# Optimization experiments

Measured on AMD Instinct MI355X. Metric: run time of the kernel, lower is better.

Reference implementation:

```python
import jax, jax.numpy as jnp
import numpy as np
import math

B, S, H, D = 4, 2048, 16, 64
HID = H * D  # 1024


def setup_inputs() -> dict:
    key = jax.random.key(0)
    ks = jax.random.split(key, 9)
    s_in = 1.0 / math.sqrt(D)
    s_hid = 1.0 / math.sqrt(HID)
    return {
        "x": jax.random.normal(ks[0], (B, S, D), dtype=jnp.float32),
        "Wq": jax.random.uniform(ks[1], (D, HID), jnp.float32, -s_in, s_in),
        "bq": jax.random.uniform(ks[2], (HID,), jnp.float32, -s_in, s_in),
        "Wk": jax.random.uniform(ks[3], (D, HID), jnp.float32, -s_in, s_in),
        "bk": jax.random.uniform(ks[4], (HID,), jnp.float32, -s_in, s_in),
        "Wv": jax.random.uniform(ks[5], (D, HID), jnp.float32, -s_in, s_in),
        "bv": jax.random.uniform(ks[6], (HID,), jnp.float32, -s_in, s_in),
        "Wo": jax.random.uniform(ks[7], (HID, D), jnp.float32, -s_hid, s_hid),
        "bo": jax.random.uniform(ks[8], (D,), jnp.float32, -s_hid, s_hid),
    }


def reference(x, Wq, bq, Wk, bk, Wv, bv, Wo, bo):
    b, s, _ = x.shape
    # projections: [B,S,D] -> [B,S,HID] -> [B,H,S,D]
    q = (x @ Wq + bq).reshape(b, s, H, D).transpose(0, 2, 1, 3)
    k = (x @ Wk + bk).reshape(b, s, H, D).transpose(0, 2, 1, 3)
    v = (x @ Wv + bv).reshape(b, s, H, D).transpose(0, 2, 1, 3)
    scores = jnp.einsum("bhqd,bhkd->bhqk", q, k) / math.sqrt(D)
    # causal mask: -inf strictly above the diagonal
    causal = jnp.tril(jnp.ones((s, s), dtype=bool))
    scores = jnp.where(causal, scores, -jnp.inf)
    attn = jax.nn.softmax(scores, axis=-1)  # dropout is identity at eval
    out = jnp.einsum("bhqk,bhkd->bhqd", attn, v)
    out = out.transpose(0, 2, 1, 3).reshape(b, s, HID)
    return out @ Wo + bo  # [B,S,D]
```

## Files before the change

kernel.cpp:

```cpp
#include <hip/hip_runtime.h>
#include <hip/hip_bf16.h>

#define B 4
#define S 2048
#define H 16
#define D 64
#define HID 1024

typedef __hip_bfloat16 bf16;
typedef __attribute__((ext_vector_type(8))) short bf16x8;
typedef __attribute__((ext_vector_type(4))) short bf16x4;
typedef __attribute__((ext_vector_type(4))) float f32x4;

static __device__ __forceinline__ float b2f(bf16 v) { return __bfloat162float(v); }

static __device__ __forceinline__ unsigned pkbf(float a, float b) {
    union { bf16 h; unsigned short u; } ua, ub;
    ua.h = __float2bfloat16(a);
    ub.h = __float2bfloat16(b);
    return (unsigned)ua.u | ((unsigned)ub.u << 16);
}

#define SCL 0.18033688011112042f

#define QSTR 72
#define VTS  132

__global__ __launch_bounds__(256) void qkv_mfma_kernel(
    const float* __restrict__ x,
    const float* __restrict__ Wq, const float* __restrict__ bq,
    const float* __restrict__ Wk, const float* __restrict__ bk,
    const float* __restrict__ Wv, const float* __restrict__ bv,
    bf16* __restrict__ q, bf16* __restrict__ k, bf16* __restrict__ v)
{
    __shared__ __align__(16) char smem[36864];
    __shared__ float bs[128];
    bf16* Xs = (bf16*)smem;
    bf16* Wt = (bf16*)(smem + 128 * QSTR * 2);

    const int tid = threadIdx.x;
    const int mat = blockIdx.y >> 3;
    const int N0  = (blockIdx.y & 7) * 128;
    const int m0  = blockIdx.x * 128;

    const float* W    = (mat == 0) ? Wq : (mat == 1) ? Wk : Wv;
    const float* bias = (mat == 0) ? bq : (mat == 1) ? bk : bv;
    bf16*        dst  = (mat == 0) ? q  : (mat == 1) ? k  : v;
    const float  oscale = (mat == 0) ? SCL : 1.0f;

    #pragma unroll
    for (int i = 0; i < 8; ++i) {
        int item = i * 256 + tid;
        int row = item >> 4, f4 = item & 15;
        float4 xv = *(const float4*)&x[(size_t)(m0 + row) * D + f4 * 4];
        union { bf16 h[4]; bf16x4 v4; } u;
        u.h[0] = __float2bfloat16(xv.x); u.h[1] = __float2bfloat16(xv.y);
        u.h[2] = __float2bfloat16(xv.z); u.h[3] = __float2bfloat16(xv.w);
        *(bf16x4*)&Xs[row * QSTR + f4 * 4] = u.v4;
    }
    #pragma unroll
    for (int i = 0; i < 2; ++i) {
        int unit = i * 256 + tid;
        int n0 = (unit & 31) * 4, k0 = (unit >> 5) * 4;
        float wv[4][4];
        #pragma unroll
        for (int j = 0; j < 4; ++j) {
            float4 t = *(const float4*)&W[(size_t)(k0 + j) * HID + N0 + n0];
            wv[j][0] = t.x; wv[j][1] = t.y; wv[j][2] = t.z; wv[j][3] = t.w;
        }
        #pragma unroll
        for (int dn = 0; dn < 4; ++dn) {
            union { bf16 h[4]; bf16x4 v4; } u;
            #pragma unroll
            for (int j = 0; j < 4; ++j) u.h[j] = __float2bfloat16(wv[j][dn]);
            *(bf16x4*)&Wt[(n0 + dn) * QSTR + k0] = u.v4;
        }
    }
    if (tid < 128) bs[tid] = bias[N0 + tid];
    __syncthreads();

    const int lane = tid & 63, wave = tid >> 6;
    const int c = lane & 15, quad = lane >> 4;

    bf16x8 af[2][2];
    #pragma unroll
    for (int mg = 0; mg < 2; ++mg)
        #pragma unroll
        for (int kc = 0; kc < 2; ++kc)
            af[mg][kc] = *(const bf16x8*)&Xs[(wave * 32 + mg * 16 + c) * QSTR + kc * 32 + quad * 8];

    f32x4 acc[2][8];
    #pragma unroll
    for (int mg = 0; mg < 2; ++mg)
        #pragma unroll
        for (int ng = 0; ng < 8; ++ng)
            acc[mg][ng] = (f32x4){0.f, 0.f, 0.f, 0.f};

    #pragma unroll
    for (int ng = 0; ng < 8; ++ng) {
        bf16x8 bf0 = *(const bf16x8*)&Wt[(ng * 16 + c) * QSTR + quad * 8];
        bf16x8 bf1 = *(const bf16x8*)&Wt[(ng * 16 + c) * QSTR + 32 + quad * 8];
        #pragma unroll
        for (int mg = 0; mg < 2; ++mg) {
            acc[mg][ng] = __builtin_amdgcn_mfma_f32_16x16x32_bf16(af[mg][0], bf0, acc[mg][ng], 0, 0, 0);
            acc[mg][ng] = __builtin_amdgcn_mfma_f32_16x16x32_bf16(af[mg][1], bf1, acc[mg][ng], 0, 0, 0);
        }
    }

    if (mat == 2) {
        bf16* T = (bf16*)smem;
        __syncthreads();
        #pragma unroll
        for (int ng = 0; ng < 8; ++ng) {
            int hid_l = ng * 16 + c;
            float bb_ = bs[hid_l];
            #pragma unroll
            for (int mg = 0; mg < 2; ++mg) {
                int ss_l = wave * 32 + mg * 16 + quad * 4;
                union { bf16 h4[4]; bf16x4 v4; } u;
                #pragma unroll
                for (int r = 0; r < 4; ++r)
                    u.h4[r] = __float2bfloat16(acc[mg][ng][r] + bb_);
                *(bf16x4*)&T[hid_l * VTS + ss_l] = u.v4;
            }
        }
        __syncthreads();
        const int b_ = m0 >> 11, ss0 = m0 & (S - 1);
        #pragma unroll
        for (int pass = 0; pass < 8; ++pass) {
            int unit = pass * 256 + tid;
            int dd_l = unit >> 4, u8 = unit & 15;
            bf16x8 val = *(const bf16x8*)&T[dd_l * VTS + u8 * 8];
            int h = (N0 >> 6) + (dd_l >> 6), ddg = dd_l & 63;
            *(bf16x8*)&dst[((size_t)(b_ * H + h) * D + ddg) * S + ss0 + u8 * 8] = val;
        }
    } else {
        bf16* T2 = (bf16*)smem;
        __syncthreads();
        #pragma unroll
        for (int ng = 0; ng < 8; ++ng) {
            int n_l = ng * 16 + c;
            float bb_ = bs[n_l];
            #pragma unroll
            for (int mg = 0; mg < 2; ++mg) {
                int row0 = wave * 32 + mg * 16 + quad * 4;
                #pragma unroll
                for (int r = 0; r < 4; ++r)
                    T2[(row0 + r) * VTS + n_l] =
                        __float2bfloat16((acc[mg][ng][r] + bb_) * oscale);
            }
        }
        __syncthreads();
        const int b_ = m0 >> 11, ss0 = m0 & (S - 1);
        #pragma unroll
        for (int pass = 0; pass < 8; ++pass) {
            int unit = pass * 256 + tid;
            int row_l = unit >> 4, n8 = unit & 15;
            bf16x8 val = *(const bf16x8*)&T2[row_l * VTS + n8 * 8];
            int n_g = N0 + n8 * 8;
            int h = n_g >> 6, dd = n_g & 63;
            *(bf16x8*)&dst[((size_t)(b_ * H + h) * S + ss0 + row_l) * D + dd] = val;
        }
    }
}

#define BT   64
#define NT   (S / BT)
#define KSTR 72
#define PST  72

__global__ __launch_bounds__(256) void flash_mfma_kernel(
    const bf16* __restrict__ qg, const bf16* __restrict__ kg,
    const bf16* __restrict__ vg, bf16* __restrict__ og)
{
    __shared__ bf16 Ks[BT * KSTR];
    __shared__ bf16 Vt[BT * KSTR];
    __shared__ bf16 PsB[4][16 * PST];
    __shared__ bf16 PsA[4][16 * PST];

    const int tid  = threadIdx.x;
    const int wave = tid >> 6;
    const int lane = tid & 63;
    const int c    = lane & 15;
    const int quad = lane >> 4;

    const int L    = (int)blockIdx.x + 16 * (int)blockIdx.y;
    const int xcd  = L & 7;
    const int slot = L >> 3;
    const int pair = slot & 15;
    const int bh   = xcd * 8 + (slot >> 4);
    const int b_   = bh >> 4, h_ = bh & 15;
    const size_t hbase = (size_t)bh * S * D;
    bf16* myPB = &PsB[wave][0];
    bf16* myPA = &PsA[wave][0];
    const int srow = wave * 16 + c;

    const int qta = pair;
    const int qtb = NT - 1 - pair;

    const int sr0 = tid >> 3,         sc0 = (tid & 7) * 8;
    const int sr1 = (tid + 256) >> 3, sc1 = sc0;

    bf16x8 qfa0, qfa1, qfb0, qfb1;
    {
        const size_t ra = hbase + (size_t)(qta * BT + srow) * D;
        const size_t rb = hbase + (size_t)(qtb * BT + srow) * D;
        qfa0 = *(const bf16x8*)(qg + ra + quad * 8);
        qfa1 = *(const bf16x8*)(qg + ra + 32 + quad * 8);
        qfb0 = *(const bf16x8*)(qg + rb + quad * 8);
        qfb1 = *(const bf16x8*)(qg + rb + 32 + quad * 8);
    }

    bf16x8 kreg0, kreg1, vreg0, vreg1;
    kreg0 = *(const bf16x8*)(kg + hbase + (size_t)sr0 * D + sc0);
    kreg1 = *(const bf16x8*)(kg + hbase + (size_t)sr1 * D + sc1);
    vreg0 = *(const bf16x8*)(vg + hbase + (size_t)sr0 * S + sc0);
    vreg1 = *(const bf16x8*)(vg + hbase + (size_t)sr1 * S + sc1);

    float la = 0.f, lb = 0.f;
    f32x4 ota[4], otb[4];
    #pragma unroll
    for (int jn = 0; jn < 4; ++jn) {
        ota[jn] = (f32x4){0.f, 0.f, 0.f, 0.f};
        otb[jn] = (f32x4){0.f, 0.f, 0.f, 0.f};
    }

    auto front = [&](bf16x8 qf0, bf16x8 qf1, bf16* Pdst, float& l1, bool diag) {
        f32x4 st[4];
        #pragma unroll
        for (int jn = 0; jn < 4; ++jn) {
            bf16x8 kf0 = *(const bf16x8*)&Ks[(jn * 16 + c) * KSTR + quad * 8];
            bf16x8 kf1 = *(const bf16x8*)&Ks[(jn * 16 + c) * KSTR + 32 + quad * 8];
            f32x4 s = {0.f, 0.f, 0.f, 0.f};
            s = __builtin_amdgcn_mfma_f32_16x16x32_bf16(kf0, qf0, s, 0, 0, 0);
            s = __builtin_amdgcn_mfma_f32_16x16x32_bf16(kf1, qf1, s, 0, 0, 0);
            st[jn] = s;
        }
        #pragma unroll
        for (int jn = 0; jn < 4; ++jn) {
            float p0 = __builtin_amdgcn_exp2f(st[jn][0]);
            float p1 = __builtin_amdgcn_exp2f(st[jn][1]);
            float p2 = __builtin_amdgcn_exp2f(st[jn][2]);
            float p3 = __builtin_amdgcn_exp2f(st[jn][3]);
            if (diag) {
                int col = jn * 16 + quad * 4;
                if (col     > srow) p0 = 0.f;
                if (col + 1 > srow) p1 = 0.f;
                if (col + 2 > srow) p2 = 0.f;
                if (col + 3 > srow) p3 = 0.f;
            }
            l1 += (p0 + p1) + (p2 + p3);
            uint2 pk;
            pk.x = pkbf(p0, p1);
            pk.y = pkbf(p2, p3);
            *(uint2*)&Pdst[c * PST + jn * 16 + quad * 4] = pk;
        }
    };
    auto pv = [&](const bf16* Psrc, f32x4* ot) {
        #pragma unroll
        for (int kc = 0; kc < 2; ++kc) {
            bf16x8 pf = *(const bf16x8*)&Psrc[c * PST + kc * 32 + quad * 8];
            #pragma unroll
            for (int jn = 0; jn < 4; ++jn) {
                bf16x8 vf = *(const bf16x8*)&Vt[(jn * 16 + c) * KSTR + kc * 32 + quad * 8];
                ot[jn] = __builtin_amdgcn_mfma_f32_16x16x32_bf16(vf, pf, ot[jn], 0, 0, 0);
            }
        }
    };

    for (int kt = 0; kt <= qtb; ++kt) {
        __syncthreads();
        *(bf16x8*)&Ks[sr0 * KSTR + sc0] = kreg0;
        *(bf16x8*)&Ks[sr1 * KSTR + sc1] = kreg1;
        *(bf16x8*)&Vt[sr0 * KSTR + sc0] = vreg0;
        *(bf16x8*)&Vt[sr1 * KSTR + sc1] = vreg1;
        __syncthreads();

        if (kt < qtb) {
            const int nb = (kt + 1) * BT;
            kreg0 = *(const bf16x8*)(kg + hbase + (size_t)(nb + sr0) * D + sc0);
            kreg1 = *(const bf16x8*)(kg + hbase + (size_t)(nb + sr1) * D + sc1);
            vreg0 = *(const bf16x8*)(vg + hbase + (size_t)sr0 * S + nb + sc0);
            vreg1 = *(const bf16x8*)(vg + hbase + (size_t)sr1 * S + nb + sc1);
        }

        const bool withA = (kt <= qta);
        front(qfb0, qfb1, myPB, lb, kt == qtb);
        if (withA) front(qfa0, qfa1, myPA, la, kt == qta);
        asm volatile("s_waitcnt lgkmcnt(0)" ::: "memory");
        pv(myPB, otb);
        if (withA) pv(myPA, ota);
    }

    {
        float lt = lb;
        lt += __shfl_xor(lt, 16);
        lt += __shfl_xor(lt, 32);
        const float inv = 1.f / lt;
        const size_t obase = ((size_t)(b_ * S + qtb * BT + srow)) * HID + h_ * 64 + quad * 4;
        #pragma unroll
        for (int jn = 0; jn < 4; ++jn) {
            union { bf16 h4[4]; bf16x4 v4; } u;
            #pragma unroll
            for (int r = 0; r < 4; ++r)
                u.h4[r] = __float2bfloat16(otb[jn][r] * inv);
            *(bf16x4*)&og[obase + jn * 16] = u.v4;
        }
    }
    {
        float lt = la;
        lt += __shfl_xor(lt, 16);
        lt += __shfl_xor(lt, 32);
        const float inv = 1.f / lt;
        const size_t obase = ((size_t)(b_ * S + qta * BT + srow)) * HID + h_ * 64 + quad * 4;
        #pragma unroll
        for (int jn = 0; jn < 4; ++jn) {
            union { bf16 h4[4]; bf16x4 v4; } u;
            #pragma unroll
            for (int r = 0; r < 4; ++r)
                u.h4[r] = __float2bfloat16(ota[jn][r] * inv);
            *(bf16x4*)&og[obase + jn * 16] = u.v4;
        }
    }
}

__global__ __launch_bounds__(256) void out_proj_mfma_kernel(
    const bf16* __restrict__ o, const float* __restrict__ Wo,
    const float* __restrict__ bo, float* __restrict__ out)
{
    __shared__ bf16 Os[32 * QSTR];
    __shared__ bf16 Wot[64 * QSTR];
    __shared__ float bos[64];

    const int tid = threadIdx.x;
    const int m0  = blockIdx.x * 32;
    const int lane = tid & 63, wave = tid >> 6;
    const int c = lane & 15, quad = lane >> 4;
    const int mtile = wave >> 1;
    const int ngb   = (wave & 1) * 2;

    const int orow = tid >> 3, ooct = tid & 7;
    const int n0 = (tid & 15) * 4, kk0 = (tid >> 4) * 4;

    if (tid < 64) bos[tid] = bo[tid];

    bf16x8 oreg = *(const bf16x8*)(o + (size_t)(m0 + orow) * HID + ooct * 8);
    float4 w4[4];
    #pragma unroll
    for (int j = 0; j < 4; ++j)
        w4[j] = *(const float4*)&Wo[(size_t)(kk0 + j) * 64 + n0];

    f32x4 acc[2];
    acc[0] = (f32x4){0.f, 0.f, 0.f, 0.f};
    acc[1] = (f32x4){0.f, 0.f, 0.f, 0.f};

    for (int chunk = 0; chunk < 16; ++chunk) {
        __syncthreads();
        *(bf16x8*)&Os[orow * QSTR + ooct * 8] = oreg;
        #pragma unroll
        for (int dn = 0; dn < 4; ++dn) {
            union { bf16 h[4]; bf16x4 v4; } u;
            u.h[0] = __float2bfloat16((&w4[0].x)[dn]);
            u.h[1] = __float2bfloat16((&w4[1].x)[dn]);
            u.h[2] = __float2bfloat16((&w4[2].x)[dn]);
            u.h[3] = __float2bfloat16((&w4[3].x)[dn]);
            *(bf16x4*)&Wot[(n0 + dn) * QSTR + kk0] = u.v4;
        }
        __syncthreads();

        if (chunk < 15) {
            const int k1 = (chunk + 1) * 64;
            oreg = *(const bf16x8*)(o + (size_t)(m0 + orow) * HID + k1 + ooct * 8);
            #pragma unroll
            for (int j = 0; j < 4; ++j)
                w4[j] = *(const float4*)&Wo[(size_t)(k1 + kk0 + j) * 64 + n0];
        }

        bf16x8 a0 = *(const bf16x8*)&Os[(mtile * 16 + c) * QSTR + quad * 8];
        bf16x8 a1 = *(const bf16x8*)&Os[(mtile * 16 + c) * QSTR + 32 + quad * 8];
        #pragma unroll
        for (int g = 0; g < 2; ++g) {
            int ng = ngb + g;
            bf16x8 b0 = *(const bf16x8*)&Wot[(ng * 16 + c) * QSTR + quad * 8];
            bf16x8 b1 = *(const bf16x8*)&Wot[(ng * 16 + c) * QSTR + 32 + quad * 8];
            acc[g] = __builtin_amdgcn_mfma_f32_16x16x32_bf16(a0, b0, acc[g], 0, 0, 0);
            acc[g] = __builtin_amdgcn_mfma_f32_16x16x32_bf16(a1, b1, acc[g], 0, 0, 0);
        }
    }

    #pragma unroll
    for (int g = 0; g < 2; ++g) {
        int n = (ngb + g) * 16 + c;
        float bb_ = bos[n];
        #pragma unroll
        for (int r = 0; r < 4; ++r) {
            int row = m0 + mtile * 16 + quad * 4 + r;
            out[(size_t)row * 64 + n] = acc[g][r] + bb_;
        }
    }
}

extern "C" void kernel_launch(void* const* d_in, const int* in_sizes, int n_in,
                              void* d_out, int out_size, void* d_ws, size_t ws_size,
                              hipStream_t stream)
{
    const float* x  = (const float*)d_in[0];
    const float* Wq = (const float*)d_in[1];
    const float* bq = (const float*)d_in[2];
    const float* Wk = (const float*)d_in[3];
    const float* bk = (const float*)d_in[4];
    const float* Wv = (const float*)d_in[5];
    const float* bv = (const float*)d_in[6];
    const float* Wo = (const float*)d_in[7];
    const float* bo = (const float*)d_in[8];

    char* ws = (char*)d_ws;
    const size_t qkv_bytes = (size_t)B * S * HID * sizeof(bf16);
    bf16* qw = (bf16*)(ws);
    bf16* kw = (bf16*)(ws + qkv_bytes);
    bf16* vw = (bf16*)(ws + 2 * qkv_bytes);
    bf16* ow = (bf16*)(ws + 3 * qkv_bytes);

    qkv_mfma_kernel<<<dim3(B * S / 128, 24), 256, 0, stream>>>(
        x, Wq, bq, Wk, bk, Wv, bv, qw, kw, vw);

    flash_mfma_kernel<<<dim3(NT / 2, B * H), 256, 0, stream>>>(qw, kw, vw, ow);

    out_proj_mfma_kernel<<<dim3(B * S / 32), 256, 0, stream>>>(ow, Wo, bo,
                                                               (float*)d_out);
}
```

Measured before the change: 172.8 us.

## Fuse paired query-tile QK and PV loops to share K/V fragments, add MFMA priority

When both query tiles A and B are active, the QK^T and PV steps for the two tiles now run in one fused loop. Each K and V fragment read from LDS is used for both tiles' MFMAs, which halves LDS fragment loads and interleaves independent MFMA chains. s_setprio raises wave priority around MFMA sections, and launch bounds now request 4 blocks per CU. The risk is higher register pressure under the occupancy bound, which could cause spills.

After: 220.9 us. +27.9%, slower.

```diff
diff --git a/kernel.cpp b/kernel.cpp
--- a/kernel.cpp
+++ b/kernel.cpp
@@ -169,7 +169,7 @@
 #define KSTR 72
 #define PST  72
 
-__global__ __launch_bounds__(256) void flash_mfma_kernel(
+__global__ __launch_bounds__(256, 4) void flash_mfma_kernel(
     const bf16* __restrict__ qg, const bf16* __restrict__ kg,
     const bf16* __restrict__ vg, bf16* __restrict__ og)
 {
@@ -227,6 +227,7 @@
 
     auto front = [&](bf16x8 qf0, bf16x8 qf1, bf16* Pdst, float& l1, bool diag) {
         f32x4 st[4];
+        __builtin_amdgcn_s_setprio(1);
         #pragma unroll
         for (int jn = 0; jn < 4; ++jn) {
             bf16x8 kf0 = *(const bf16x8*)&Ks[(jn * 16 + c) * KSTR + quad * 8];
@@ -236,6 +237,7 @@
             s = __builtin_amdgcn_mfma_f32_16x16x32_bf16(kf1, qf1, s, 0, 0, 0);
             st[jn] = s;
         }
+        __builtin_amdgcn_s_setprio(0);
         #pragma unroll
         for (int jn = 0; jn < 4; ++jn) {
             float p0 = __builtin_amdgcn_exp2f(st[jn][0]);
@@ -256,7 +258,54 @@
             *(uint2*)&Pdst[c * PST + jn * 16 + quad * 4] = pk;
         }
     };
+
+    auto front2 = [&](bool diagA) {
+        #pragma unroll
+        for (int jn = 0; jn < 4; ++jn) {
+            bf16x8 kf0 = *(const bf16x8*)&Ks[(jn * 16 + c) * KSTR + quad * 8];
+            bf16x8 kf1 = *(const bf16x8*)&Ks[(jn * 16 + c) * KSTR + 32 + quad * 8];
+            f32x4 sb = {0.f, 0.f, 0.f, 0.f};
+            f32x4 sa = {0.f, 0.f, 0.f, 0.f};
+            __builtin_amdgcn_s_setprio(1);
+            sb = __builtin_amdgcn_mfma_f32_16x16x32_bf16(kf0, qfb0, sb, 0, 0, 0);
+            sb = __builtin_amdgcn_mfma_f32_16x16x32_bf16(kf1, qfb1, sb, 0, 0, 0);
+            sa = __builtin_amdgcn_mfma_f32_16x16x32_bf16(kf0, qfa0, sa, 0, 0, 0);
+            sa = __builtin_amdgcn_mfma_f32_16x16x32_bf16(kf1, qfa1, sa, 0, 0, 0);
+            __builtin_amdgcn_s_setprio(0);
+            {
+                float p0 = __builtin_amdgcn_exp2f(sb[0]);
+                float p1 = __builtin_amdgcn_exp2f(sb[1]);
+                float p2 = __builtin_amdgcn_exp2f(sb[2]);
+                float p3 = __builtin_amdgcn_exp2f(sb[3]);
+                lb += (p0 + p1) + (p2 + p3);
+                uint2 pk;
+                pk.x = pkbf(p0, p1);
+                pk.y = pkbf(p2, p3);
+                *(uint2*)&myPB[c * PST + jn * 16 + quad * 4] = pk;
+            }
+            {
+                float p0 = __builtin_amdgcn_exp2f(sa[0]);
+                float p1 = __builtin_amdgcn_exp2f(sa[1]);
+                float p2 = __builtin_amdgcn_exp2f(sa[2]);
+                float p3 = __builtin_amdgcn_exp2f(sa[3]);
+                if (diagA) {
+                    int col = jn * 16 + quad * 4;
+                    if (col     > srow) p0 = 0.f;
+                    if (col + 1 > srow) p1 = 0.f;
+                    if (col + 2 > srow) p2 = 0.f;
+                    if (col + 3 > srow) p3 = 0.f;
+                }
+                la += (p0 + p1) + (p2 + p3);
+                uint2 pk;
+                pk.x = pkbf(p0, p1);
+                pk.y = pkbf(p2, p3);
+                *(uint2*)&myPA[c * PST + jn * 16 + quad * 4] = pk;
+            }
+        }
+    };
+
     auto pv = [&](const bf16* Psrc, f32x4* ot) {
+        __builtin_amdgcn_s_setprio(1);
         #pragma unroll
         for (int kc = 0; kc < 2; ++kc) {
             bf16x8 pf = *(const bf16x8*)&Psrc[c * PST + kc * 32 + quad * 8];
@@ -266,6 +315,7 @@
                 ot[jn] = __builtin_amdgcn_mfma_f32_16x16x32_bf16(vf, pf, ot[jn], 0, 0, 0);
             }
         }
+        __builtin_amdgcn_s_setprio(0);
     };
 
     for (int kt = 0; kt <= qtb; ++kt) {
@@ -284,12 +334,27 @@
             vreg1 = *(const bf16x8*)(vg + hbase + (size_t)sr1 * S + nb + sc1);
         }
 
-        const bool withA = (kt <= qta);
-        front(qfb0, qfb1, myPB, lb, kt == qtb);
-        if (withA) front(qfa0, qfa1, myPA, la, kt == qta);
-        asm volatile("s_waitcnt lgkmcnt(0)" ::: "memory");
-        pv(myPB, otb);
-        if (withA) pv(myPA, ota);
+        if (kt <= qta) {
+            front2(kt == qta);
+            asm volatile("s_waitcnt lgkmcnt(0)" ::: "memory");
+            __builtin_amdgcn_s_setprio(1);
+            #pragma unroll
+            for (int kc = 0; kc < 2; ++kc) {
+                bf16x8 pfb = *(const bf16x8*)&myPB[c * PST + kc * 32 + quad * 8];
+                bf16x8 pfa = *(const bf16x8*)&myPA[c * PST + kc * 32 + quad * 8];
+                #pragma unroll
+                for (int jn = 0; jn < 4; ++jn) {
+                    bf16x8 vf = *(const bf16x8*)&Vt[(jn * 16 + c) * KSTR + kc * 32 + quad * 8];
+                    otb[jn] = __builtin_amdgcn_mfma_f32_16x16x32_bf16(vf, pfb, otb[jn], 0, 0, 0);
+                    ota[jn] = __builtin_amdgcn_mfma_f32_16x16x32_bf16(vf, pfa, ota[jn], 0, 0, 0);
+                }
+            }
+            __builtin_amdgcn_s_setprio(0);
+        } else {
+            front(qfb0, qfb1, myPB, lb, kt == qtb);
+            asm volatile("s_waitcnt lgkmcnt(0)" ::: "memory");
+            pv(myPB, otb);
+        }
     }
 
     {
```

## Double-buffer K/V tiles with XOR-swizzled LDS and a single P scratch

Applied to the files above, without the earlier changes.

The flash attention kernel now keeps two LDS buffers for K and V, so the next tile is stored while the current one is consumed. This needs one barrier per iteration instead of two, and global prefetch runs two tiles ahead. The padded row strides are replaced by an XOR swizzle on 8-element groups to avoid bank conflicts without padding. The two per-wave P buffers become one, with the B and A query tiles processed one after the other, which serializes their front/PV phases and reduces instruction-level overlap.

New measurement: 163.8 us. -5.2%, faster.

```diff
diff --git a/kernel.cpp b/kernel.cpp
--- a/kernel.cpp
+++ b/kernel.cpp
@@ -166,17 +166,14 @@
 
 #define BT   64
 #define NT   (S / BT)
-#define KSTR 72
-#define PST  72
 
 __global__ __launch_bounds__(256) void flash_mfma_kernel(
     const bf16* __restrict__ qg, const bf16* __restrict__ kg,
     const bf16* __restrict__ vg, bf16* __restrict__ og)
 {
-    __shared__ bf16 Ks[BT * KSTR];
-    __shared__ bf16 Vt[BT * KSTR];
-    __shared__ bf16 PsB[4][16 * PST];
-    __shared__ bf16 PsA[4][16 * PST];
+    __shared__ bf16 Ks[2][BT * 64];
+    __shared__ bf16 Vt[2][BT * 64];
+    __shared__ bf16 Ps[4][16 * 64];
 
     const int tid  = threadIdx.x;
     const int wave = tid >> 6;
@@ -191,15 +188,18 @@
     const int bh   = xcd * 8 + (slot >> 4);
     const int b_   = bh >> 4, h_ = bh & 15;
     const size_t hbase = (size_t)bh * S * D;
-    bf16* myPB = &PsB[wave][0];
-    bf16* myPA = &PsA[wave][0];
+    bf16* myP = &Ps[wave][0];
     const int srow = wave * 16 + c;
 
     const int qta = pair;
     const int qtb = NT - 1 - pair;
 
-    const int sr0 = tid >> 3,         sc0 = (tid & 7) * 8;
-    const int sr1 = (tid + 256) >> 3, sc1 = sc0;
+    const int sr0 = tid >> 3, g0 = tid & 7;
+    const int sr1 = sr0 + 32;
+    const int sc0 = g0 * 8;
+    const int so0 = sr0 * 64 + ((g0 ^ (sr0 & 7)) << 3);
+    const int so1 = sr1 * 64 + ((g0 ^ (sr1 & 7)) << 3);
+    const int cx7 = c & 7;
 
     bf16x8 qfa0, qfa1, qfb0, qfb1;
     {
@@ -211,12 +211,6 @@
         qfb1 = *(const bf16x8*)(qg + rb + 32 + quad * 8);
     }
 
-    bf16x8 kreg0, kreg1, vreg0, vreg1;
-    kreg0 = *(const bf16x8*)(kg + hbase + (size_t)sr0 * D + sc0);
-    kreg1 = *(const bf16x8*)(kg + hbase + (size_t)sr1 * D + sc1);
-    vreg0 = *(const bf16x8*)(vg + hbase + (size_t)sr0 * S + sc0);
-    vreg1 = *(const bf16x8*)(vg + hbase + (size_t)sr1 * S + sc1);
-
     float la = 0.f, lb = 0.f;
     f32x4 ota[4], otb[4];
     #pragma unroll
@@ -225,12 +219,13 @@
         otb[jn] = (f32x4){0.f, 0.f, 0.f, 0.f};
     }
 
-    auto front = [&](bf16x8 qf0, bf16x8 qf1, bf16* Pdst, float& l1, bool diag) {
+    auto front = [&](const bf16* Kb, bf16x8 qf0, bf16x8 qf1, float& l1, bool diag) {
         f32x4 st[4];
         #pragma unroll
         for (int jn = 0; jn < 4; ++jn) {
-            bf16x8 kf0 = *(const bf16x8*)&Ks[(jn * 16 + c) * KSTR + quad * 8];
-            bf16x8 kf1 = *(const bf16x8*)&Ks[(jn * 16 + c) * KSTR + 32 + quad * 8];
+            const int rb_ = (jn * 16 + c) * 64;
+            bf16x8 kf0 = *(const bf16x8*)&Kb[rb_ + ((quad       ^ cx7) << 3)];
+            bf16x8 kf1 = *(const bf16x8*)&Kb[rb_ + (((quad + 4) ^ cx7) << 3)];
             f32x4 s = {0.f, 0.f, 0.f, 0.f};
             s = __builtin_amdgcn_mfma_f32_16x16x32_bf16(kf0, qf0, s, 0, 0, 0);
             s = __builtin_amdgcn_mfma_f32_16x16x32_bf16(kf1, qf1, s, 0, 0, 0);
@@ -253,43 +248,71 @@
             uint2 pk;
             pk.x = pkbf(p0, p1);
             pk.y = pkbf(p2, p3);
-            *(uint2*)&Pdst[c * PST + jn * 16 + quad * 4] = pk;
+            *(uint2*)&myP[c * 64 + (((2 * jn + (quad >> 1)) ^ cx7) << 3) + (quad & 1) * 4] = pk;
         }
     };
-    auto pv = [&](const bf16* Psrc, f32x4* ot) {
+    auto pv = [&](const bf16* Vb, f32x4* ot) {
         #pragma unroll
         for (int kc = 0; kc < 2; ++kc) {
-            bf16x8 pf = *(const bf16x8*)&Psrc[c * PST + kc * 32 + quad * 8];
+            bf16x8 pf = *(const bf16x8*)&myP[c * 64 + (((kc * 4 + quad) ^ cx7) << 3)];
             #pragma unroll
             for (int jn = 0; jn < 4; ++jn) {
-                bf16x8 vf = *(const bf16x8*)&Vt[(jn * 16 + c) * KSTR + kc * 32 + quad * 8];
+                const int rb_ = (jn * 16 + c) * 64;
+                bf16x8 vf = *(const bf16x8*)&Vb[rb_ + (((kc * 4 + quad) ^ cx7) << 3)];
                 ot[jn] = __builtin_amdgcn_mfma_f32_16x16x32_bf16(vf, pf, ot[jn], 0, 0, 0);
             }
         }
     };
 
+    bf16x8 kreg0, kreg1, vreg0, vreg1;
+    kreg0 = *(const bf16x8*)(kg + hbase + (size_t)sr0 * D + sc0);
+    kreg1 = *(const bf16x8*)(kg + hbase + (size_t)sr1 * D + sc0);
+    vreg0 = *(const bf16x8*)(vg + hbase + (size_t)sr0 * S + sc0);
+    vreg1 = *(const bf16x8*)(vg + hbase + (size_t)sr1 * S + sc0);
+    *(bf16x8*)&Ks[0][so0] = kreg0;
+    *(bf16x8*)&Ks[0][so1] = kreg1;
+    *(bf16x8*)&Vt[0][so0] = vreg0;
+    *(bf16x8*)&Vt[0][so1] = vreg1;
+    {
+        const int nb = BT;
+        kreg0 = *(const bf16x8*)(kg + hbase + (size_t)(nb + sr0) * D + sc0);
+        kreg1 = *(const bf16x8*)(kg + hbase + (size_t)(nb + sr1) * D + sc0);
+        vreg0 = *(const bf16x8*)(vg + hbase + (size_t)sr0 * S + nb + sc0);
+        vreg1 = *(const bf16x8*)(vg + hbase + (size_t)sr1 * S + nb + sc0);
+    }
+    __syncthreads();
+
+    int cur = 0;
     for (int kt = 0; kt <= qtb; ++kt) {
-        __syncthreads();
-        *(bf16x8*)&Ks[sr0 * KSTR + sc0] = kreg0;
-        *(bf16x8*)&Ks[sr1 * KSTR + sc1] = kreg1;
-        *(bf16x8*)&Vt[sr0 * KSTR + sc0] = vreg0;
-        *(bf16x8*)&Vt[sr1 * KSTR + sc1] = vreg1;
-        __syncthreads();
-
         if (kt < qtb) {
-            const int nb = (kt + 1) * BT;
-            kreg0 = *(const bf16x8*)(kg + hbase + (size_t)(nb + sr0) * D + sc0);
-            kreg1 = *(const bf16x8*)(kg + hbase + (size_t)(nb + sr1) * D + sc1);
-            vreg0 = *(const bf16x8*)(vg + hbase + (size_t)sr0 * S + nb + sc0);
-            vreg1 = *(const bf16x8*)(vg + hbase + (size_t)sr1 * S + nb + sc1);
-        }
-
-        const bool withA = (kt <= qta);
-        front(qfb0, qfb1, myPB, lb, kt == qtb);
-        if (withA) front(qfa0, qfa1, myPA, la, kt == qta);
+            *(bf16x8*)&Ks[cur ^ 1][so0] = kreg0;
+            *(bf16x8*)&Ks[cur ^ 1][so1] = kreg1;
+            *(bf16x8*)&Vt[cur ^ 1][so0] = vreg0;
+            *(bf16x8*)&Vt[cur ^ 1][so1] = vreg1;
+            if (kt + 1 < qtb) {
+                const int nb = (kt + 2) * BT;
+                kreg0 = *(const bf16x8*)(kg + hbase + (size_t)(nb + sr0) * D + sc0);
+                kreg1 = *(const bf16x8*)(kg + hbase + (size_t)(nb + sr1) * D + sc0);
+                vreg0 = *(const bf16x8*)(vg + hbase + (size_t)sr0 * S + nb + sc0);
+                vreg1 = *(const bf16x8*)(vg + hbase + (size_t)sr1 * S + nb + sc0);
+            }
+        }
+
+        const bf16* Kb = &Ks[cur][0];
+        const bf16* Vb = &Vt[cur][0];
+        front(Kb, qfb0, qfb1, lb, kt == qtb);
         asm volatile("s_waitcnt lgkmcnt(0)" ::: "memory");
-        pv(myPB, otb);
-        if (withA) pv(myPA, ota);
+        pv(Vb, otb);
+        if (kt <= qta) {
+            front(Kb, qfa0, qfa1, la, kt == qta);
+            asm volatile("s_waitcnt lgkmcnt(0)" ::: "memory");
+            pv(Vb, ota);
+        }
+
+        if (kt < qtb) {
+            __syncthreads();
+            cur ^= 1;
+        }
     }
 
     {
```
